# Optimization experiments

Measured on AMD Instinct MI355X. Metric: run time of the kernel, lower is better.

## Reference

```python
import jax, jax.numpy as jnp
import numpy as np

B, C, H, W = 8, 128, 128, 128
HEADS = 8
EPS = 1e-12  # torch F.normalize default eps


def _dwconv(x, w, pad):
    # x: [B, G, H, W], w: [G, 1, k, k] depthwise kernel
    return jax.lax.conv_general_dilated(
        x, w, window_strides=(1, 1), padding=((pad, pad), (pad, pad)),
        feature_group_count=w.shape[0],
        dimension_numbers=('NCHW', 'OIHW', 'NCHW'))


def setup_inputs() -> dict:
    key = jax.random.key(0)
    ks = jax.random.split(key, 10)
    s = 0.05
    return {
        'x': jax.random.normal(ks[0], (B, C, H, W), jnp.float32),
        'w_qkv': jax.random.normal(ks[1], (3 * C, C), jnp.float32) * s,
        'w_dw3': jax.random.normal(ks[2], (3 * C, 1, 3, 3), jnp.float32) * s,
        'w_dw5': jax.random.normal(ks[3], (3 * C, 1, 5, 5), jnp.float32) * s,
        'w_dw7': jax.random.normal(ks[4], (3 * C, 1, 7, 7), jnp.float32) * s,
        'w_q': jax.random.normal(ks[5], (C, 3 * C), jnp.float32) * s,
        'w_k': jax.random.normal(ks[6], (C, 3 * C), jnp.float32) * s,
        'w_v': jax.random.normal(ks[7], (C, 3 * C), jnp.float32) * s,
        'w_out': jax.random.normal(ks[8], (C, C), jnp.float32) * s,
        'temperature': jnp.ones((HEADS, 1, 1), jnp.float32),
    }


def reference(x, w_qkv, w_dw3, w_dw5, w_dw7, w_q, w_k, w_v, w_out, temperature):
    b, c, h, w = x.shape
    heads = temperature.shape[0]
    # 1x1 qkv conv: [b, 3c, h, w]
    xq = jnp.einsum('bchw,oc->bohw', x, w_qkv)
    # multi-scale depthwise convs on the same qkv tensor
    q1, k1, v1 = jnp.split(_dwconv(xq, w_dw3, 1), 3, axis=1)
    q2, k2, v2 = jnp.split(_dwconv(xq, w_dw5, 2), 3, axis=1)
    q3, k3, v3 = jnp.split(_dwconv(xq, w_dw7, 3), 3, axis=1)
    q = jnp.einsum('bchw,oc->bohw', jnp.concatenate([q1, q2, q3], 1), w_q)
    k = jnp.einsum('bchw,oc->bohw', jnp.concatenate([k1, k2, k3], 1), w_k)
    v = jnp.einsum('bchw,oc->bohw', jnp.concatenate([v1, v2, v3], 1), w_v)
    # [b, head, c_head, h*w]
    dh = c // heads
    q = q.reshape(b, heads, dh, h * w)
    k = k.reshape(b, heads, dh, h * w)
    v = v.reshape(b, heads, dh, h * w)
    # L2 normalize along spatial dim
    q = q / jnp.maximum(jnp.linalg.norm(q, axis=-1, keepdims=True), EPS)
    k = k / jnp.maximum(jnp.linalg.norm(k, axis=-1, keepdims=True), EPS)
    # channel attention: [b, head, c_head, c_head]
    attn = jnp.einsum('bhcn,bhdn->bhcd', q, k) * temperature
    attn = jax.nn.softmax(attn, axis=-1)
    out = jnp.einsum('bhcd,bhdn->bhcn', attn, v).reshape(b, c, h, w)
    return jnp.einsum('bchw,oc->bohw', out, w_out)
```

## Files before the change

### kernel.cpp

```cpp
#include <hip/hip_runtime.h>
#include <hip/hip_bf16.h>

#define NB 8
#define NSP 16384

typedef unsigned short u16;
typedef __attribute__((ext_vector_type(8))) short short8_;
typedef __attribute__((ext_vector_type(8))) unsigned short u16x8;
typedef __attribute__((ext_vector_type(4))) float f32x4;
typedef __attribute__((ext_vector_type(4))) unsigned u32x4;

__device__ __forceinline__ float b2f(u16 u) {
  unsigned v = ((unsigned)u) << 16;
  float f;
  __builtin_memcpy(&f, &v, 4);
  return f;
}
__device__ __forceinline__ u16 f2b(float f) {
  __hip_bfloat16 h = __float2bfloat16(f);
  u16 u;
  __builtin_memcpy(&u, &h, 2);
  return u;
}
__device__ __forceinline__ float ldf(const void* p, size_t i, int isbf) {
  return isbf ? b2f(((const u16*)p)[i]) : ((const float*)p)[i];
}

__global__ __launch_bounds__(256) void prep_all(
    const void* __restrict__ wq, const void* __restrict__ wk,
    const void* __restrict__ wqkv, const void* __restrict__ wv,
    const void* __restrict__ wdw3, const void* __restrict__ wdw5,
    const void* __restrict__ wdw7, const void* __restrict__ temp,
    u16* __restrict__ Wqf, u16* __restrict__ Wkf, u16* __restrict__ Wkvf,
    u16* __restrict__ Wbv, float* __restrict__ Wdww,
    int* __restrict__ flag, float* __restrict__ Sz)
{
  const int isbf = (((const u16*)temp)[0] != 0) ? 1 : 0;
  const int bx = blockIdx.x;
  const int tid = threadIdx.x;

  if (bx < 72) {
    int i = bx * 256 + tid;
    if (i == 0) *flag = isbf;
    if (i < 18432) Sz[i] = 0.f;
  } else if (bx < 144) {
    const int mb = bx - 72;
    const int mat = mb / 24;
    const int fi = (mb - mat * 24) * 256 + tid;
    const int lane = fi & 63, m = (fi >> 6) & 7, ks = (fi >> 9) & 3, blk = fi >> 11;
    const int quad = lane >> 4, col = lane & 15;
    const void* src;
    u16* dst;
    size_t so;
    if (mat == 2) {
      so = (size_t)(blk * 128 + m * 16 + col) * 128 + ks * 32 + quad * 8;
      src = wqkv; dst = Wkvf;
    } else {
      so = (size_t)(m * 16 + col) * 384 + blk * 128 + ks * 32 + quad * 8;
      src = mat ? wk : wq; dst = mat ? Wkf : Wqf;
    }
    if (isbf) {
      *(u16x8*)&dst[(size_t)fi * 8] = *(const u16x8*)((const u16*)src + so);
    } else {
      f32x4 a = *(const f32x4*)((const float*)src + so);
      f32x4 b = *(const f32x4*)((const float*)src + so + 4);
      u16 us[8];
#pragma unroll
      for (int j = 0; j < 4; j++) { us[j] = f2b(a[j]); us[4 + j] = f2b(b[j]); }
      *(u16x8*)&dst[(size_t)fi * 8] = *(u16x8*)us;
    }
  } else if (bx < 336) {
    int i = (bx - 144) * 256 + tid;
    Wbv[i] = isbf ? ((const u16*)wv)[i] : f2b(((const float*)wv)[i]);
  } else {
    int i = (bx - 336) * 256 + tid;
    int gc = i / 84, t = i - gc * 84;
    float v = 0.f;
    if (t < 9)       v = ldf(wdw3, (size_t)gc * 9 + t, isbf);
    else if (t < 34) v = ldf(wdw5, (size_t)gc * 25 + (t - 9), isbf);
    else if (t < 83) v = ldf(wdw7, (size_t)gc * 49 + (t - 34), isbf);
    Wdww[i] = v;
  }
}

__global__ __launch_bounds__(256) void gemm_mfma(
    const u16* __restrict__ Wb,
    const void* __restrict__ X,
    u16* __restrict__ C, long c_bstride, int M,
    const int* __restrict__ flagp)
{
  const int isbf = *flagp;
  __shared__ u16 Xs[128 * 76];
  __shared__ u16 Cs[128 * 72];
  const int b = blockIdx.z;
  const int n0 = blockIdx.x * 64;
  const int tid = threadIdx.x;
  const size_t xbase = (size_t)b * 2097152 + n0;

  if (isbf) {
    const u16* Xp = (const u16*)X;
#pragma unroll
    for (int i = 0; i < 4; i++) {
      int s = i * 256 + tid;
      int kk = s >> 3, p = (s & 7) * 8;
      u32x4 v = *(const u32x4*)(Xp + xbase + (size_t)kk * NSP + p);
      uint2 lo; lo.x = v[0]; lo.y = v[1];
      uint2 hi; hi.x = v[2]; hi.y = v[3];
      *(uint2*)&Xs[kk * 76 + p]     = lo;
      *(uint2*)&Xs[kk * 76 + p + 4] = hi;
    }
  } else {
    const float* Xp = (const float*)X;
#pragma unroll
    for (int i = 0; i < 4; i++) {
      int s = i * 256 + tid;
      int kk = s >> 3, p = (s & 7) * 8;
      f32x4 fa = *(const f32x4*)(Xp + xbase + (size_t)kk * NSP + p);
      f32x4 fb = *(const f32x4*)(Xp + xbase + (size_t)kk * NSP + p + 4);
      u16 u8v[8];
#pragma unroll
      for (int j = 0; j < 4; j++) u8v[j] = f2b(fa[j]);
#pragma unroll
      for (int j = 0; j < 4; j++) u8v[4 + j] = f2b(fb[j]);
      *(uint2*)&Xs[kk * 76 + p]     = *(uint2*)&u8v[0];
      *(uint2*)&Xs[kk * 76 + p + 4] = *(uint2*)&u8v[4];
    }
  }
  __syncthreads();

  const int wid = tid >> 6, lane = tid & 63;
  const int quad = lane >> 4, col = lane & 15;
  const int nw = wid * 16;
  u16* Cb = C + (size_t)b * c_bstride + n0;
  const short8_* Af = (const short8_*)Wb;

  for (int ob = 0; ob < M; ob += 128) {
    const int obi = ob >> 7;
    f32x4 z = {0.f, 0.f, 0.f, 0.f};
    f32x4 acc[8];
#pragma unroll
    for (int m = 0; m < 8; m++) acc[m] = z;

#pragma unroll
    for (int ks = 0; ks < 4; ks++) {
      const int k0 = ks * 32;
      short8_ bfrag;
#pragma unroll
      for (int j = 0; j < 8; j++)
        bfrag[j] = (short)Xs[(k0 + quad * 8 + j) * 76 + nw + col];
#pragma unroll
      for (int m = 0; m < 8; m++) {
        short8_ afrag = Af[(size_t)(((obi * 4 + ks) * 8 + m) * 64 + lane)];
        acc[m] = __builtin_amdgcn_mfma_f32_16x16x32_bf16(afrag, bfrag, acc[m], 0, 0, 0);
      }
    }

    if (ob) __syncthreads();
#pragma unroll
    for (int m = 0; m < 8; m++)
#pragma unroll
      for (int r = 0; r < 4; r++)
        Cs[(m * 16 + quad * 4 + r) * 72 + nw + col] = f2b(acc[m][r]);
    __syncthreads();
#pragma unroll
    for (int i = 0; i < 4; i++) {
      int u = i * 256 + tid;
      int row = u >> 3, off = (u & 7) * 8;
      u16x8 v = *(const u16x8*)&Cs[row * 72 + off];
      *(u16x8*)(Cb + (size_t)(ob + row) * NSP + off) = v;
    }
  }
}

__global__ __launch_bounds__(256) void convgemm(
    const u16* __restrict__ xqg, long x_bstride, long x_gstride, int gc_base0,
    const float* __restrict__ Wdww,
    const u16* __restrict__ Afrag, long a_bstride, long a_gstride,
    void* __restrict__ Out, long out_gstride, int om,
    const int* __restrict__ flagp)
{
  const int isbf = *flagp;
  __shared__ u16 regA[7680];
  __shared__ float dww[2688];
  u16* in_s = regA;
  u16* Bp = regA;
  const int b = blockIdx.z, g = blockIdx.y;
  const int t0 = blockIdx.x;
  const int t = ((t0 & 7) << 5) | (t0 >> 3);
  const int y0 = (t >> 3) * 4, x0 = (t & 7) * 16;
  const u16* xb = xqg + (size_t)b * x_bstride + (size_t)g * x_gstride;
  const short8_* Af = (const short8_*)(Afrag + (size_t)b * a_bstride + (size_t)g * a_gstride);
  const int gc_base = gc_base0 + g * 128;
  const int tid = threadIdx.x;
  const int cc_t = tid >> 3;
  const int py_t = (tid >> 1) & 3;
  const int xh   = tid & 1;
  const int wid = tid >> 6, lane = tid & 63;
  const int quad = lane >> 4, col = lane & 15;

  const int hy  = lane / 6;
  const int hc4 = lane - hy * 6;
  const int gy_s = y0 - 3 + hy, gx_s = x0 - 4 + hc4 * 4;
  const bool sval = (lane < 60);
  const bool gok = sval && ((unsigned)gy_s < 128u) && ((unsigned)gx_s <= 124u);
  const u16* gsrc0 = xb + (size_t)wid * NSP + (gy_s * 128 + gx_s);
  const int ldso = wid * 240 + hy * 24 + hc4 * 4;

  uint2 hreg[8];

#pragma unroll
  for (int i = 0; i < 8; i++) {
    uint2 v; v.x = 0u; v.y = 0u;
    if (gok) v = *(const uint2*)(gsrc0 + (size_t)(i * 4) * NSP);
    hreg[i] = v;
  }

  f32x4 z = {0.f, 0.f, 0.f, 0.f};
  f32x4 acc[8];
#pragma unroll
  for (int m = 0; m < 8; m++) acc[m] = z;

  for (int chn = 0; chn < 4; chn++) {
    const int c0 = chn * 32;
    if (chn) __syncthreads();

    if (sval) {
#pragma unroll
      for (int i = 0; i < 8; i++)
        *(uint2*)&in_s[ldso + i * 960] = hreg[i];
    }
    {
      const float* wg = Wdww + (size_t)(gc_base + c0) * 84;
#pragma unroll
      for (int i = 0; i < 3; i++) {
        int s = i * 256 + tid;
        if (s < 672) *(f32x4*)&dww[s * 4] = *(const f32x4*)(wg + s * 4);
      }
    }
    __syncthreads();

    if (chn < 3) {
      const u16* gsrc = gsrc0 + (size_t)(c0 + 32) * NSP;
#pragma unroll
      for (int i = 0; i < 8; i++) {
        uint2 v; v.x = 0u; v.y = 0u;
        if (gok) v = *(const uint2*)(gsrc + (size_t)(i * 4) * NSP);
        hreg[i] = v;
      }
    }

    float a0[8], a1[8], a2[8];
#pragma unroll
    for (int px = 0; px < 8; px++) { a0[px] = 0.f; a1[px] = 0.f; a2[px] = 0.f; }
    {
      const float* dwc = dww + cc_t * 84;
      const u16* rowbase = in_s + cc_t * 240 + xh * 8;
#pragma unroll
      for (int dy = 0; dy < 7; dy++) {
        const u16* rp = rowbase + (py_t + dy) * 24;
        u32x4 ra = *(const u32x4*)rp;
        u32x4 rb = *(const u32x4*)(rp + 8);
        float row[14];
#pragma unroll
        for (int j = 0; j < 14; j++) {
          int l = j + 1;
          unsigned wd = (l < 8) ? ra[l >> 1] : rb[(l >> 1) - 4];
          unsigned bits = (l & 1) ? (wd & 0xffff0000u) : (wd << 16);
          __builtin_memcpy(&row[j], &bits, 4);
        }
#pragma unroll
        for (int dx = 0; dx < 7; dx++) {
          float wv = dwc[34 + dy * 7 + dx];
#pragma unroll
          for (int px = 0; px < 8; px++) a2[px] += row[px + dx] * wv;
        }
        if (dy >= 1 && dy <= 5) {
          int dy5 = dy - 1;
#pragma unroll
          for (int dx = 0; dx < 5; dx++) {
            float wv = dwc[9 + dy5 * 5 + dx];
#pragma unroll
            for (int px = 0; px < 8; px++) a1[px] += row[px + 1 + dx] * wv;
          }
        }
        if (dy >= 2 && dy <= 4) {
          int dy3 = dy - 2;
#pragma unroll
          for (int dx = 0; dx < 3; dx++) {
            float wv = dwc[dy3 * 3 + dx];
#pragma unroll
            for (int px = 0; px < 8; px++) a0[px] += row[px + 2 + dx] * wv;
          }
        }
      }
    }
    __syncthreads();

    {
      const int pb = py_t * 16 + xh * 8;
      u16 us[8];
#pragma unroll
      for (int px = 0; px < 8; px++) us[px] = f2b(a0[px]);
      *(uint2*)&Bp[(0 * 32 + cc_t) * 68 + pb]     = *(uint2*)&us[0];
      *(uint2*)&Bp[(0 * 32 + cc_t) * 68 + pb + 4] = *(uint2*)&us[4];
#pragma unroll
      for (int px = 0; px < 8; px++) us[px] = f2b(a1[px]);
      *(uint2*)&Bp[(1 * 32 + cc_t) * 68 + pb]     = *(uint2*)&us[0];
      *(uint2*)&Bp[(1 * 32 + cc_t) * 68 + pb + 4] = *(uint2*)&us[4];
#pragma unroll
      for (int px = 0; px < 8; px++) us[px] = f2b(a2[px]);
      *(uint2*)&Bp[(2 * 32 + cc_t) * 68 + pb]     = *(uint2*)&us[0];
      *(uint2*)&Bp[(2 * 32 + cc_t) * 68 + pb + 4] = *(uint2*)&us[4];
    }
    __syncthreads();

#pragma unroll
    for (int s = 0; s < 3; s++) {
      const int k0 = s * 32;
      short8_ bfrag;
#pragma unroll
      for (int j = 0; j < 8; j++)
        bfrag[j] = (short)Bp[(k0 + quad * 8 + j) * 68 + wid * 16 + col];
#pragma unroll
      for (int m = 0; m < 8; m++) {
        short8_ afrag = Af[(size_t)(((s * 4 + chn) * 8 + m) * 64 + lane)];
        acc[m] = __builtin_amdgcn_mfma_f32_16x16x32_bf16(afrag, bfrag, acc[m], 0, 0, 0);
      }
    }
  }

#pragma unroll
  for (int m = 0; m < 8; m++)
#pragma unroll
    for (int r = 0; r < 4; r++) {
      int o = m * 16 + quad * 4 + r;
      int ng = (y0 + wid) * 128 + x0 + col;
      size_t base = ((size_t)b * 128 + o) * NSP + ng;
      if (om && !isbf) ((float*)Out)[base] = acc[m][r];
      else ((u16*)Out + (size_t)g * out_gstride)[base] = f2b(acc[m][r]);
    }
}

__global__ __launch_bounds__(256) void s_mfma(
    const u16* __restrict__ qb, const u16* __restrict__ kb,
    float* __restrict__ S, float* __restrict__ qs, float* __restrict__ ks)
{
  __shared__ u16 Qs[16 * 520];
  __shared__ u16 Ks[16 * 520];
  const int chunk = blockIdx.x, h = blockIdx.y, b = blockIdx.z;
  const int tid = threadIdx.x;
  const int n0 = chunk * 512;
  const size_t gbase = ((size_t)b * 128 + h * 16) * NSP + n0;

#pragma unroll
  for (int i = 0; i < 4; i++) {
    int idx = i * 256 + tid;
    int row = idx >> 6, off = (idx & 63) * 8;
    *(u16x8*)&Qs[row * 520 + off] = *(const u16x8*)(qb + gbase + (size_t)row * NSP + off);
    *(u16x8*)&Ks[row * 520 + off] = *(const u16x8*)(kb + gbase + (size_t)row * NSP + off);
  }
  __syncthreads();

  const int wid = tid >> 6, lane = tid & 63;
  const int quad = lane >> 4, col = lane & 15;
  const int nb = wid * 128;
  f32x4 acc = {0.f, 0.f, 0.f, 0.f};
  float sq = 0.f, sk = 0.f;
#pragma unroll
  for (int k2 = 0; k2 < 4; k2++) {
    int off = nb + k2 * 32 + quad * 8;
    short8_ qf = *(const short8_*)&Qs[col * 520 + off];
    short8_ kf = *(const short8_*)&Ks[col * 520 + off];
#pragma unroll
    for (int j = 0; j < 8; j++) {
      float qv = b2f((u16)qf[j]), kv = b2f((u16)kf[j]);
      sq += qv * qv; sk += kv * kv;
    }
    acc = __builtin_amdgcn_mfma_f32_16x16x32_bf16(qf, kf, acc, 0, 0, 0);
  }

  sq += __shfl_xor(sq, 16); sq += __shfl_xor(sq, 32);
  sk += __shfl_xor(sk, 16); sk += __shfl_xor(sk, 32);
  if (quad == 0) {
    atomicAdd(&qs[b * 128 + h * 16 + col], sq);
    atomicAdd(&ks[b * 128 + h * 16 + col], sk);
  }

  __syncthreads();
  float* Sred = (float*)Qs;
#pragma unroll
  for (int r = 0; r < 4; r++)
    Sred[wid * 256 + (quad * 4 + r) * 16 + col] = acc[r];
  __syncthreads();
  {
    float v = Sred[tid] + Sred[256 + tid] + Sred[512 + tid] + Sred[768 + tid];
    atomicAdd(&S[((size_t)(b * 8 + h) << 8) + tid], v);
  }
}

__global__ __launch_bounds__(256) void fold_wv(
    const u16* __restrict__ Mmat, const u16* __restrict__ Wbv,
    u16* __restrict__ Wmv)
{
  const int b = blockIdx.y, jb = blockIdx.x;
  const u16* Mb = Mmat + (size_t)b * 16384;
  const int t = threadIdx.x;
  const int o = t >> 1, jh = t & 1;
  const int j0 = jb * 32 + jh * 16;
  float acc[16];
#pragma unroll
  for (int jj = 0; jj < 16; jj++) acc[jj] = 0.f;
  for (int d = 0; d < 128; d++) {
    float mv = b2f(Mb[o * 128 + d]);
    const u16* wr = Wbv + (size_t)d * 384 + j0;
#pragma unroll
    for (int jj = 0; jj < 16; jj++) acc[jj] += mv * b2f(wr[jj]);
  }
  const int kc = j0 >> 7, ks = (j0 >> 5) & 3, q0 = (j0 >> 3) & 3;
  const int m = o >> 4, col = o & 15;
  u16* outb = Wmv + (size_t)b * 49152;
  const int fi0 = ((kc * 4 + ks) * 8 + m) * 64 + q0 * 16 + col;
  u16x8 v8;
#pragma unroll
  for (int jj = 0; jj < 8; jj++) v8[jj] = f2b(acc[jj]);
  *(u16x8*)&outb[(size_t)fi0 * 8] = v8;
#pragma unroll
  for (int jj = 0; jj < 8; jj++) v8[jj] = f2b(acc[8 + jj]);
  *(u16x8*)&outb[(size_t)(fi0 + 16) * 8] = v8;
}

__global__ __launch_bounds__(256) void attn_mat(
    const float* __restrict__ S, const float* __restrict__ qs,
    const float* __restrict__ ks,
    const void* __restrict__ w_out, const void* __restrict__ temp,
    u16* __restrict__ Mmat, const int* __restrict__ flagp)
{
  const int isbf = *flagp;
  const int b = blockIdx.x;
  __shared__ float attn_s[8 * 16 * 16];
  const int t = threadIdx.x;
  if (t < 128) {
    int h = t >> 4, c = t & 15;
    float qn = fmaxf(sqrtf(fmaxf(qs[b * 128 + h * 16 + c], 0.f)), 1e-12f);
    float tm = ldf(temp, h, isbf);
    float zv[16];
    float m = -1e30f;
    for (int d = 0; d < 16; d++) {
      float kn = fmaxf(sqrtf(fmaxf(ks[b * 128 + h * 16 + d], 0.f)), 1e-12f);
      zv[d] = S[(((size_t)b * 8 + h) * 16 + c) * 16 + d] / (qn * kn) * tm;
      m = fmaxf(m, zv[d]);
    }
    float sum = 0.f;
    for (int d = 0; d < 16; d++) { zv[d] = expf(zv[d] - m); sum += zv[d]; }
    float inv = 1.f / sum;
    for (int d = 0; d < 16; d++) attn_s[(h * 16 + c) * 16 + d] = zv[d] * inv;
  }
  __syncthreads();
  for (int idx = t; idx < 128 * 128; idx += 256) {
    int o = idx >> 7, cp = idx & 127;
    int h = cp >> 4, e = cp & 15;
    float a = 0.f;
    for (int d = 0; d < 16; d++)
      a += ldf(w_out, (size_t)o * 128 + h * 16 + d, isbf) * attn_s[(h * 16 + d) * 16 + e];
    Mmat[(size_t)b * 16384 + idx] = f2b(a);
  }
}

extern "C" void kernel_launch(void* const* d_in, const int* in_sizes, int n_in,
                              void* d_out, int out_size, void* d_ws, size_t ws_size,
                              hipStream_t stream) {
  const void* x     = d_in[0];
  const void* w_qkv = d_in[1];
  const void* w_dw3 = d_in[2];
  const void* w_dw5 = d_in[3];
  const void* w_dw7 = d_in[4];
  const void* w_q   = d_in[5];
  const void* w_k   = d_in[6];
  const void* w_v   = d_in[7];
  const void* w_o   = d_in[8];
  const void* temp  = d_in[9];

  char* ws = (char*)d_ws;
  u16* dsc = (u16*)d_out;
  u16* Wbqf  = dsc;
  u16* Wbkf  = dsc + 49152;
  u16* Wbkvf = dsc + 98304;

  u16* xq    = (u16*)ws;
  u16* q     = (u16*)(ws + 100663296);
  char* tail = ws + 167772160;
  float* S   = (float*)tail;
  float* qs  = (float*)(tail + 65536);
  float* ks  = (float*)(tail + 69632);
  int* flag  = (int*)(tail + 73728);
  u16* Mmat  = (u16*)(tail + 73856);
  u16* Wbv   = (u16*)(tail + 336000);
  u16* Wmv   = (u16*)(tail + 434304);
  float* Wdww = (float*)(tail + 1220736);
  u16* k     = q + 16777216;

  prep_all<<<462, 256, 0, stream>>>(
      w_q, w_k, w_qkv, w_v, w_dw3, w_dw5, w_dw7, temp,
      Wbqf, Wbkf, Wbkvf, Wbv, Wdww, flag, S);

  gemm_mfma<<<dim3(256, 1, NB), 256, 0, stream>>>(
      Wbkvf, x, xq, 384L * NSP, 384, flag);

  convgemm<<<dim3(256, 2, NB), 256, 0, stream>>>(
      xq, 384L * NSP, 128L * NSP, 0, Wdww,
      Wbqf, 0, 49152, q, 16777216L, 0, flag);

  s_mfma<<<dim3(32, 8, NB), 256, 0, stream>>>(q, k, S, qs, ks);

  attn_mat<<<NB, 256, 0, stream>>>(S, qs, ks, w_o, temp, Mmat, flag);
  fold_wv<<<dim3(12, NB), 256, 0, stream>>>(Mmat, Wbv, Wmv);

  convgemm<<<dim3(256, 1, NB), 256, 0, stream>>>(
      xq + 256L * NSP, 384L * NSP, 0, 256, Wdww,
      Wmv, 49152, 0, d_out, 0, 1, flag);
}
```

Measured before the change: 481.4 us.

## Store qkv intermediate as fp16 and compute depthwise convs with packed fdot2

The qkv GEMM output is now written as fp16 instead of bf16, and the depthwise conv weights are pre-packed into fp16 pairs in two alignments (even and odd). The multi-scale depthwise conv inner loop then uses v_dot2_f32_f16 on packed pixel pairs instead of unpacking to fp32 and doing scalar FMAs. This halves the ALU instruction count of the conv stage and removes the bf16-to-fp32 unpack work, at the cost of fp16 range and precision on the intermediate activations and weights. The packed weight table is slightly larger in shared memory.

Result: slower. 527.7 us (+9.6%).

```diff
diff --git a/kernel.cpp b/kernel.cpp
--- a/kernel.cpp
+++ b/kernel.cpp
@@ -9,6 +9,7 @@
 typedef __attribute__((ext_vector_type(8))) unsigned short u16x8;
 typedef __attribute__((ext_vector_type(4))) float f32x4;
 typedef __attribute__((ext_vector_type(4))) unsigned u32x4;
+typedef __attribute__((ext_vector_type(2))) _Float16 h16x2;
 
 __device__ __forceinline__ float b2f(u16 u) {
   unsigned v = ((unsigned)u) << 16;
@@ -22,8 +23,20 @@
   __builtin_memcpy(&u, &h, 2);
   return u;
 }
+__device__ __forceinline__ u16 f2h(float f) {
+  _Float16 h = (_Float16)f;
+  u16 u;
+  __builtin_memcpy(&u, &h, 2);
+  return u;
+}
 __device__ __forceinline__ float ldf(const void* p, size_t i, int isbf) {
   return isbf ? b2f(((const u16*)p)[i]) : ((const float*)p)[i];
+}
+__device__ __forceinline__ float fdot2u(unsigned a, unsigned b, float c) {
+  h16x2 x, y;
+  __builtin_memcpy(&x, &a, 4);
+  __builtin_memcpy(&y, &b, 4);
+  return __builtin_amdgcn_fdot2(x, y, c, false);
 }
 
 __global__ __launch_bounds__(256) void prep_all(
@@ -32,7 +45,7 @@
     const void* __restrict__ wdw3, const void* __restrict__ wdw5,
     const void* __restrict__ wdw7, const void* __restrict__ temp,
     u16* __restrict__ Wqf, u16* __restrict__ Wkf, u16* __restrict__ Wkvf,
-    u16* __restrict__ Wbv, float* __restrict__ Wdww,
+    u16* __restrict__ Wbv, unsigned* __restrict__ Wdwp,
     int* __restrict__ flag, float* __restrict__ Sz)
 {
   const int isbf = (((const u16*)temp)[0] != 0) ? 1 : 0;
@@ -74,12 +87,48 @@
     Wbv[i] = isbf ? ((const u16*)wv)[i] : f2b(((const float*)wv)[i]);
   } else {
     int i = (bx - 336) * 256 + tid;
-    int gc = i / 84, t = i - gc * 84;
-    float v = 0.f;
-    if (t < 9)       v = ldf(wdw3, (size_t)gc * 9 + t, isbf);
-    else if (t < 34) v = ldf(wdw5, (size_t)gc * 25 + (t - 9), isbf);
-    else if (t < 83) v = ldf(wdw7, (size_t)gc * 49 + (t - 34), isbf);
-    Wdww[i] = v;
+    if (i < 39936) {
+      int gc = i / 104, t = i - gc * 104;
+      float lo = 0.f, hi = 0.f;
+      if (t < 56) {
+        int al = (t >= 28) ? 1 : 0;
+        int u = t - al * 28;
+        int dy = u >> 2, p = u & 3;
+        size_t base = (size_t)gc * 49 + dy * 7;
+        if (!al) {
+          lo = ldf(wdw7, base + 2 * p, isbf);
+          hi = (2 * p + 1 < 7) ? ldf(wdw7, base + 2 * p + 1, isbf) : 0.f;
+        } else {
+          lo = (p == 0) ? 0.f : ldf(wdw7, base + 2 * p - 1, isbf);
+          hi = ldf(wdw7, base + 2 * p, isbf);
+        }
+      } else if (t < 86) {
+        int al = (t >= 71) ? 1 : 0;
+        int u = t - (al ? 71 : 56);
+        int dy = u / 3, p = u % 3;
+        size_t base = (size_t)gc * 25 + dy * 5;
+        if (!al) {
+          lo = ldf(wdw5, base + 2 * p, isbf);
+          hi = (2 * p + 1 < 5) ? ldf(wdw5, base + 2 * p + 1, isbf) : 0.f;
+        } else {
+          lo = (p == 0) ? 0.f : ldf(wdw5, base + 2 * p - 1, isbf);
+          hi = ldf(wdw5, base + 2 * p, isbf);
+        }
+      } else if (t < 98) {
+        int al = (t >= 92) ? 1 : 0;
+        int u = t - (al ? 92 : 86);
+        int dy = u >> 1, p = u & 1;
+        size_t base = (size_t)gc * 9 + dy * 3;
+        if (!al) {
+          lo = ldf(wdw3, base + 2 * p, isbf);
+          hi = (2 * p + 1 < 3) ? ldf(wdw3, base + 2 * p + 1, isbf) : 0.f;
+        } else {
+          lo = (p == 0) ? 0.f : ldf(wdw3, base + 2 * p - 1, isbf);
+          hi = ldf(wdw3, base + 2 * p, isbf);
+        }
+      }
+      Wdwp[i] = (unsigned)f2h(lo) | ((unsigned)f2h(hi) << 16);
+    }
   }
 }
 
@@ -160,7 +209,7 @@
     for (int m = 0; m < 8; m++)
 #pragma unroll
       for (int r = 0; r < 4; r++)
-        Cs[(m * 16 + quad * 4 + r) * 72 + nw + col] = f2b(acc[m][r]);
+        Cs[(m * 16 + quad * 4 + r) * 72 + nw + col] = f2h(acc[m][r]);
     __syncthreads();
 #pragma unroll
     for (int i = 0; i < 4; i++) {
@@ -174,14 +223,14 @@
 
 __global__ __launch_bounds__(256) void convgemm(
     const u16* __restrict__ xqg, long x_bstride, long x_gstride, int gc_base0,
-    const float* __restrict__ Wdww,
+    const unsigned* __restrict__ Wdwp,
     const u16* __restrict__ Afrag, long a_bstride, long a_gstride,
     void* __restrict__ Out, long out_gstride, int om,
     const int* __restrict__ flagp)
 {
   const int isbf = *flagp;
   __shared__ u16 regA[7680];
-  __shared__ float dww[2688];
+  __shared__ unsigned dwp[3328];
   u16* in_s = regA;
   u16* Bp = regA;
   const int b = blockIdx.z, g = blockIdx.y;
@@ -207,7 +256,6 @@
   const int ldso = wid * 240 + hy * 24 + hc4 * 4;
 
   uint2 hreg[8];
-
 #pragma unroll
   for (int i = 0; i < 8; i++) {
     uint2 v; v.x = 0u; v.y = 0u;
@@ -230,11 +278,11 @@
         *(uint2*)&in_s[ldso + i * 960] = hreg[i];
     }
     {
-      const float* wg = Wdww + (size_t)(gc_base + c0) * 84;
-#pragma unroll
-      for (int i = 0; i < 3; i++) {
+      const u32x4* wg = (const u32x4*)(Wdwp + (size_t)(gc_base + c0) * 104);
+#pragma unroll
+      for (int i = 0; i < 4; i++) {
         int s = i * 256 + tid;
-        if (s < 672) *(f32x4*)&dww[s * 4] = *(const f32x4*)(wg + s * 4);
+        if (s < 832) ((u32x4*)dwp)[s] = wg[s];
       }
     }
     __syncthreads();
@@ -253,43 +301,65 @@
 #pragma unroll
     for (int px = 0; px < 8; px++) { a0[px] = 0.f; a1[px] = 0.f; a2[px] = 0.f; }
     {
-      const float* dwc = dww + cc_t * 84;
+      const unsigned* wch = dwp + cc_t * 104;
       const u16* rowbase = in_s + cc_t * 240 + xh * 8;
 #pragma unroll
       for (int dy = 0; dy < 7; dy++) {
         const u16* rp = rowbase + (py_t + dy) * 24;
         u32x4 ra = *(const u32x4*)rp;
         u32x4 rb = *(const u32x4*)(rp + 8);
-        float row[14];
-#pragma unroll
-        for (int j = 0; j < 14; j++) {
-          int l = j + 1;
-          unsigned wd = (l < 8) ? ra[l >> 1] : rb[(l >> 1) - 4];
-          unsigned bits = (l & 1) ? (wd & 0xffff0000u) : (wd << 16);
-          __builtin_memcpy(&row[j], &bits, 4);
-        }
-#pragma unroll
-        for (int dx = 0; dx < 7; dx++) {
-          float wv = dwc[34 + dy * 7 + dx];
-#pragma unroll
-          for (int px = 0; px < 8; px++) a2[px] += row[px + dx] * wv;
+        unsigned W[8];
+#pragma unroll
+        for (int j = 0; j < 4; j++) { W[j] = ra[j]; W[4 + j] = rb[j]; }
+        {
+          const unsigned* A2w = wch + dy * 4;
+          const unsigned* B2w = wch + 28 + dy * 4;
+#pragma unroll
+          for (int e = 0; e < 4; e++) {
+            float s = a2[2 * e];
+            s = fdot2u(W[e],     B2w[0], s);
+            s = fdot2u(W[e + 1], B2w[1], s);
+            s = fdot2u(W[e + 2], B2w[2], s);
+            s = fdot2u(W[e + 3], B2w[3], s);
+            a2[2 * e] = s;
+            float u = a2[2 * e + 1];
+            u = fdot2u(W[e + 1], A2w[0], u);
+            u = fdot2u(W[e + 2], A2w[1], u);
+            u = fdot2u(W[e + 3], A2w[2], u);
+            u = fdot2u(W[e + 4], A2w[3], u);
+            a2[2 * e + 1] = u;
+          }
         }
         if (dy >= 1 && dy <= 5) {
-          int dy5 = dy - 1;
-#pragma unroll
-          for (int dx = 0; dx < 5; dx++) {
-            float wv = dwc[9 + dy5 * 5 + dx];
-#pragma unroll
-            for (int px = 0; px < 8; px++) a1[px] += row[px + 1 + dx] * wv;
+          const unsigned* A1w = wch + 56 + (dy - 1) * 3;
+          const unsigned* B1w = wch + 71 + (dy - 1) * 3;
+#pragma unroll
+          for (int e = 0; e < 4; e++) {
+            float s = a1[2 * e];
+            s = fdot2u(W[e + 1], A1w[0], s);
+            s = fdot2u(W[e + 2], A1w[1], s);
+            s = fdot2u(W[e + 3], A1w[2], s);
+            a1[2 * e] = s;
+            float u = a1[2 * e + 1];
+            u = fdot2u(W[e + 1], B1w[0], u);
+            u = fdot2u(W[e + 2], B1w[1], u);
+            u = fdot2u(W[e + 3], B1w[2], u);
+            a1[2 * e + 1] = u;
           }
         }
         if (dy >= 2 && dy <= 4) {
-          int dy3 = dy - 2;
-#pragma unroll
-          for (int dx = 0; dx < 3; dx++) {
-            float wv = dwc[dy3 * 3 + dx];
-#pragma unroll
-            for (int px = 0; px < 8; px++) a0[px] += row[px + 2 + dx] * wv;
+          const unsigned* A0w = wch + 86 + (dy - 2) * 2;
+          const unsigned* B0w = wch + 92 + (dy - 2) * 2;
+#pragma unroll
+          for (int e = 0; e < 4; e++) {
+            float s = a0[2 * e];
+            s = fdot2u(W[e + 1], B0w[0], s);
+            s = fdot2u(W[e + 2], B0w[1], s);
+            a0[2 * e] = s;
+            float u = a0[2 * e + 1];
+            u = fdot2u(W[e + 2], A0w[0], u);
+            u = fdot2u(W[e + 3], A0w[1], u);
+            a0[2 * e + 1] = u;
           }
         }
       }
@@ -496,18 +566,18 @@
   u16* Mmat  = (u16*)(tail + 73856);
   u16* Wbv   = (u16*)(tail + 336000);
   u16* Wmv   = (u16*)(tail + 434304);
-  float* Wdww = (float*)(tail + 1220736);
+  unsigned* Wdwp = (unsigned*)(tail + 1220736);
   u16* k     = q + 16777216;
 
-  prep_all<<<462, 256, 0, stream>>>(
+  prep_all<<<492, 256, 0, stream>>>(
       w_q, w_k, w_qkv, w_v, w_dw3, w_dw5, w_dw7, temp,
-      Wbqf, Wbkf, Wbkvf, Wbv, Wdww, flag, S);
+      Wbqf, Wbkf, Wbkvf, Wbv, Wdwp, flag, S);
 
   gemm_mfma<<<dim3(256, 1, NB), 256, 0, stream>>>(
       Wbkvf, x, xq, 384L * NSP, 384, flag);
 
   convgemm<<<dim3(256, 2, NB), 256, 0, stream>>>(
-      xq, 384L * NSP, 128L * NSP, 0, Wdww,
+      xq, 384L * NSP, 128L * NSP, 0, Wdwp,
       Wbqf, 0, 49152, q, 16777216L, 0, flag);
 
   s_mfma<<<dim3(32, 8, NB), 256, 0, stream>>>(q, k, S, qs, ks);
@@ -516,6 +586,6 @@
   fold_wv<<<dim3(12, NB), 256, 0, stream>>>(Mmat, Wbv, Wmv);
 
   convgemm<<<dim3(256, 1, NB), 256, 0, stream>>>(
-      xq + 256L * NSP, 384L * NSP, 0, 256, Wdww,
+      xq + 256L * NSP, 384L * NSP, 0, 256, Wdwp,
       Wmv, 49152, 0, d_out, 0, 1, flag);
 }
```
